# Optimization experiments

Hardware: AMD Instinct MI355X
Metric: run time of the kernel (lower is better)

The kernel has to match this reference:

```python
import jax, jax.numpy as jnp
import numpy as np

N_ENT = 100000   # n_entities
N_REL = 64       # n_relations
E_DIM = 64       # e_dim == r_dim (rel2ent is None)
K = 32           # neighbors per entity
B = 1024         # batch of seed entities
SLOPE = 0.2      # LeakyReLU negative_slope


def _xavier(key, shape, fan_in, fan_out):
    b = (6.0 / (fan_in + fan_out)) ** 0.5
    return jax.random.uniform(key, shape, jnp.float32, -b, b)


def setup_inputs() -> dict:
    key = jax.random.key(0)
    ks = jax.random.split(key, 10)
    E = _xavier(ks[0], (N_ENT, E_DIM), N_ENT, E_DIM)          # entity_embs.weight
    R = _xavier(ks[1], (N_REL, E_DIM), N_REL, E_DIM)          # relation_embs.weight
    att_w1 = _xavier(ks[2], (E_DIM, 2 * E_DIM), 2 * E_DIM, E_DIM)  # attention[0], no bias
    att_w2 = _xavier(ks[3], (E_DIM, E_DIM), E_DIM, E_DIM)          # attention[2], no bias
    att_w3 = _xavier(ks[4], (1, E_DIM), E_DIM, 1)                  # attention[4], no bias
    wx_w = _xavier(ks[5], (E_DIM, E_DIM), E_DIM, E_DIM)            # Wx[0].weight
    wx_b = jnp.zeros((E_DIM,), jnp.float32)                        # Wx[0].bias
    wc_w = _xavier(ks[6], (E_DIM, 2 * E_DIM), 2 * E_DIM, E_DIM)    # W_concat.weight
    wc_b = jnp.zeros((E_DIM,), jnp.float32)                        # W_concat.bias
    entity_idx = jax.random.randint(ks[7], (B,), 0, N_ENT)
    adj_entity = jax.random.randint(ks[8], (N_ENT, K), 0, N_ENT)
    adj_relation = jax.random.randint(ks[9], (N_ENT, K), 0, N_REL)
    return {
        "entity_idx": entity_idx, "adj_entity": adj_entity, "adj_relation": adj_relation,
        "E": E, "R": R, "att_w1": att_w1, "att_w2": att_w2, "att_w3": att_w3,
        "wx_w": wx_w, "wx_b": wx_b, "wc_w": wc_w, "wc_b": wc_b,
    }


def _lookup(W, idx):
    # nn.Embedding(max_norm=1): rows whose L2 norm exceeds 1 are renormalized.
    e = W[idx]
    n = jnp.linalg.norm(e, axis=-1, keepdims=True)
    return e * jnp.where(n > 1.0, 1.0 / (n + 1e-7), 1.0)


def _forward(entity_idx, adj_entity, adj_relation, E, R,
             att_w1, att_w2, att_w3, wx_w, wx_b, wc_w, wc_b):
    leaky = lambda x: jnp.where(x >= 0, x, SLOPE * x)
    # attention MLP on cat([h, r]): split first linear so the broadcast h term
    # is computed once per batch row instead of materializing [B, N, 2e].
    w1h, w1r = att_w1[:, :E_DIM], att_w1[:, E_DIM:]

    def gat(h, r, t):
        # h: [B, e] (broadcast over neighbors), r,t: [B, N, e]
        hid = jax.nn.relu(jnp.einsum('be,fe->bf', h, w1h)[:, None, :]
                          + jnp.einsum('bne,fe->bnf', r, w1r))
        hid = jax.nn.relu(jnp.einsum('bnf,gf->bng', hid, att_w2))
        a = jax.nn.sigmoid(jnp.einsum('bng,og->bno', hid, att_w3)[..., 0])  # [B, N]
        w = jax.nn.softmax(a, axis=-1)
        agg = jnp.einsum('bn,bne->be', w, t)       # softmax-weighted neighbor sum
        return agg @ wx_w.T + wx_b                 # per-head Linear (n_heads=1)

    Bsz = entity_idx.shape[0]
    # hop-1 / hop-2 neighbor index gathers (get_neighbors)
    ent1 = adj_entity[entity_idx]                  # [B, K]
    rel1 = adj_relation[entity_idx]                # [B, K]
    ent2 = adj_entity[ent1].reshape(Bsz, -1)       # [B, K*K]
    rel2 = adj_relation[ent1].reshape(Bsz, -1)     # [B, K*K]

    h = _lookup(E, entity_idx)                     # [B, e]
    t1 = _lookup(E, ent1)                          # [B, K, e]
    t2 = _lookup(E, ent2)                          # [B, K*K, e]
    r1 = _lookup(R, rel1)
    r2 = _lookup(R, rel2)

    # iter 0: seed entity broadcast as head
    v1 = leaky(gat(h, r1, t1))                                      # [B, e]
    emb1 = leaky(jnp.concatenate([h, v1], -1) @ wc_w.T + wc_b)      # aggregate 'concat'
    # iter 1: summed hop-1 neighborhood as head
    hsum = t1.sum(axis=1)                                           # [B, e]
    v2 = leaky(gat(hsum, r2, t2))
    emb2 = leaky(jnp.concatenate([hsum, v2], -1) @ wc_w.T + wc_b)
    # sum_aggregator 'concat': e_u = cat(embs[2], cat(embs[1], embs[0]))
    return jnp.concatenate([emb2, emb1, h], axis=-1)                # [B, 3e]


def reference(entity_idx, adj_entity, adj_relation, E, R,
              att_w1, att_w2, att_w3, wx_w, wx_b, wc_w, wc_b):
    return _forward(entity_idx, adj_entity, adj_relation, E, R,
                    att_w1, att_w2, att_w3, wx_w, wx_b, wc_w, wc_b)
```

## Files before the change

kernel.cpp:

```cpp
#include <hip/hip_runtime.h>

#define SLOPE 0.2f

__device__ __forceinline__ float leaky(float x) { return x >= 0.f ? x : SLOPE * x; }

enum : int {
  OFF_PT   = 0,
  OFF_W2T  = OFF_PT + 4096,
  OFF_A3   = OFF_W2T + 4096,
  OFF_WXT  = OFF_A3 + 64,
  OFF_WXB  = OFF_WXT + 4096,
  OFF_WCT  = OFF_WXB + 64,
  OFF_WCB  = OFF_WCT + 8192,
  OFF_W1HT = OFF_WCB + 64,
  OFF_HQ   = OFF_W1HT + 4096,
  OFF_HSUM = OFF_HQ + 131072,
  OFF_ATAB = OFF_HSUM + 65536,
  OFF_ENT1 = OFF_ATAB + 131072,
  OFF_REL1 = OFF_ENT1 + 32768,
  WS_FLOATS = OFF_REL1 + 32768
};

__global__ __launch_bounds__(256) void k1_prep(
    const float* __restrict__ R, const float* __restrict__ w1,
    const float* __restrict__ w2, const float* __restrict__ w3,
    const float* __restrict__ wxw, const float* __restrict__ wxb,
    const float* __restrict__ wcw, const float* __restrict__ wcb,
    float* __restrict__ ws) {
  __shared__ float Rn[64 * 65];
  int tid = threadIdx.x, wv = tid >> 6, lane = tid & 63;
  for (int r = wv; r < 64; r += 4) {
    float v = R[r * 64 + lane];
    float ss = v * v;
    #pragma unroll
    for (int m = 1; m < 64; m <<= 1) ss += __shfl_xor(ss, m, 64);
    float n = sqrtf(ss);
    float sc = n > 1.f ? 1.f / (n + 1e-7f) : 1.f;
    Rn[r * 65 + lane] = v * sc;
  }
  __syncthreads();
  int gt = blockIdx.x * 256 + tid;
  for (int i = gt; i < 4096; i += 2048) {
    int f = i >> 6, r = i & 63;
    float acc = 0.f;
    #pragma unroll
    for (int e = 0; e < 64; ++e) acc += Rn[r * 65 + e] * w1[f * 128 + 64 + e];
    ws[OFF_PT + f * 64 + r] = acc;
  }
  for (int i = gt; i < 4096; i += 2048) {
    int f = i >> 6, g = i & 63;
    ws[OFF_W2T + i] = w2[g * 64 + f];
  }
  for (int i = gt; i < 4096; i += 2048) {
    int e = i >> 6, f = i & 63;
    ws[OFF_WXT + i]  = wxw[f * 64 + e];
    ws[OFF_W1HT + i] = w1[f * 128 + e];
  }
  for (int i = gt; i < 8192; i += 2048) {
    int e = i >> 6, f = i & 63;
    ws[OFF_WCT + i] = wcw[f * 128 + e];
  }
  if (gt < 64) {
    ws[OFF_A3 + gt]  = w3[gt];
    ws[OFF_WXB + gt] = wxb[gt];
    ws[OFF_WCB + gt] = wcb[gt];
  }
}

__global__ __launch_bounds__(256) void k2_stagea(
    const int* __restrict__ entity_idx, const int* __restrict__ adj_entity,
    const int* __restrict__ adj_relation, const float* __restrict__ E,
    float* __restrict__ ws) {
  __shared__ int s_ent1[32];
  __shared__ float s_h[64], s_hs[64];
  __shared__ float s_part[4][64];
  int b = blockIdx.x, tid = threadIdx.x, wv = tid >> 6, lane = tid & 63;
  int idx = entity_idx[b];
  if (tid < 64) s_h[tid] = E[(long)idx * 64 + tid];
  if (tid >= 64 && tid < 96) {
    int i = tid - 64;
    int e1 = adj_entity[(long)idx * 32 + i];
    int r1 = adj_relation[(long)idx * 32 + i];
    s_ent1[i] = e1;
    ((int*)ws)[OFF_ENT1 + b * 32 + i] = e1;
    ((int*)ws)[OFF_REL1 + b * 32 + i] = r1;
  }
  __syncthreads();
  float hs = 0.f;
  #pragma unroll
  for (int k = 0; k < 8; ++k) hs += E[(long)s_ent1[wv * 8 + k] * 64 + lane];
  s_part[wv][lane] = hs;
  __syncthreads();
  if (tid < 64) {
    float t = s_part[0][tid] + s_part[1][tid] + s_part[2][tid] + s_part[3][tid];
    s_hs[tid] = t;
    ws[OFF_HSUM + b * 64 + tid] = t;
  }
  __syncthreads();
  {
    const float* src = (wv < 2) ? s_h : s_hs;
    int e0 = (wv & 1) * 32;
    float p = 0.f;
    #pragma unroll 8
    for (int e = 0; e < 32; ++e) p += ws[OFF_W1HT + (e0 + e) * 64 + lane] * src[e0 + e];
    s_part[wv][lane] = p;
  }
  __syncthreads();
  if (tid < 64) {
    ws[OFF_HQ + (b * 2 + 0) * 64 + tid] = s_part[0][tid] + s_part[1][tid];
  } else if (tid < 128) {
    int i = tid - 64;
    ws[OFF_HQ + (b * 2 + 1) * 64 + i] = s_part[2][i] + s_part[3][i];
  }
}

__global__ __launch_bounds__(256) void k3_atab(const float* __restrict__ ws,
                                               float* __restrict__ atab) {
  __shared__ float s_hid[64 * 64];
  __shared__ float s_part[4][64];
  int g64 = blockIdx.x;
  int tid = threadIdx.x, rel = tid & 63;
  int wv = __builtin_amdgcn_readfirstlane(tid >> 6);
  const float* hq  = ws + OFF_HQ + g64 * 64;
  const float* PT  = ws + OFF_PT;
  const float* W2T = ws + OFF_W2T;
  const float* A3  = ws + OFF_A3;
  #pragma unroll
  for (int i = 0; i < 16; ++i) {
    int f = wv * 16 + i;
    s_hid[f * 64 + rel] = fmaxf(hq[f] + PT[f * 64 + rel], 0.f);
  }
  __syncthreads();
  float acc[16];
  #pragma unroll
  for (int i = 0; i < 16; ++i) acc[i] = 0.f;
  int g0 = wv * 16;
  #pragma unroll 4
  for (int f = 0; f < 64; ++f) {
    float hv = s_hid[f * 64 + rel];
    const float* w = W2T + f * 64 + g0;
    #pragma unroll
    for (int i = 0; i < 16; ++i) acc[i] += w[i] * hv;
  }
  float s = 0.f;
  #pragma unroll
  for (int i = 0; i < 16; ++i) s += A3[g0 + i] * fmaxf(acc[i], 0.f);
  s_part[wv][rel] = s;
  __syncthreads();
  if (tid < 64) {
    float t = s_part[0][tid] + s_part[1][tid] + s_part[2][tid] + s_part[3][tid];
    float a = 1.f / (1.f + __expf(-t));
    atab[g64 * 64 + tid] = __expf(a);
  }
}

__global__ __launch_bounds__(256) void k4_agg(
    const int* __restrict__ entity_idx, const int* __restrict__ adj_entity,
    const int* __restrict__ adj_relation, const float* __restrict__ E,
    const float* __restrict__ ws, float* __restrict__ out) {
  __shared__ int s_ent1[32], s_rel1[32];
  __shared__ float s_at1[64], s_at2[64];
  __shared__ int s_ei[1024];
  __shared__ float s_w[1024];
  __shared__ float s_accA[4][64];
  __shared__ float s_accB[4][64];
  __shared__ float s_agg1[64], s_agg2[64], s_v1[64], s_v2[64], s_h[64], s_hs[64];
  __shared__ float s_L1, s_L2;
  int b = blockIdx.x, tid = threadIdx.x, wv = tid >> 6, lane = tid & 63;
  int sub = lane >> 4, eg = lane & 15;
  const float4* E4 = (const float4*)E;

  if (tid < 32) {
    s_ent1[tid] = ((const int*)ws)[OFF_ENT1 + b * 32 + tid];
    s_rel1[tid] = ((const int*)ws)[OFF_REL1 + b * 32 + tid];
  }
  if (tid >= 64 && tid < 128) {
    int i = tid - 64;
    s_at1[i] = ws[OFF_ATAB + (b * 2 + 0) * 64 + i];
    s_at2[i] = ws[OFF_ATAB + (b * 2 + 1) * 64 + i];
  }
  if (tid >= 128 && tid < 192) {
    int i = tid - 128;
    s_h[i]  = E[(long)entity_idx[b] * 64 + i];
    s_hs[i] = ws[OFF_HSUM + b * 64 + i];
  }
  if (tid == 0) s_L2 = 0.f;
  __syncthreads();

  float wsum = 0.f;
  #pragma unroll
  for (int i = 0; i < 4; ++i) {
    int n = tid + i * 256;
    int j = n >> 5, i2 = n & 31;
    long base = (long)s_ent1[j] * 32 + i2;
    int ei = adj_entity[base];
    int ri = adj_relation[base];
    float wgt = s_at2[ri];
    s_ei[n] = ei;
    s_w[n] = wgt;
    wsum += wgt;
  }
  #pragma unroll
  for (int m = 1; m < 64; m <<= 1) wsum += __shfl_xor(wsum, m, 64);
  if (lane == 0) atomicAdd(&s_L2, wsum);

  if (tid < 32) {
    float w = s_at1[s_rel1[tid]];
    #pragma unroll
    for (int m = 1; m < 32; m <<= 1) w += __shfl_xor(w, m, 64);
    if (tid == 0) s_L1 = w;
  }

  {
    float4 acc = {0.f, 0.f, 0.f, 0.f};
    #pragma unroll
    for (int i = 0; i < 2; ++i) {
      int n = i * 16 + wv * 4 + sub;
      float wgt = s_at1[s_rel1[n]];
      float4 v = E4[(long)s_ent1[n] * 16 + eg];
      acc.x += wgt * v.x; acc.y += wgt * v.y; acc.z += wgt * v.z; acc.w += wgt * v.w;
    }
    #pragma unroll
    for (int m = 16; m < 64; m <<= 1) {
      acc.x += __shfl_xor(acc.x, m, 64); acc.y += __shfl_xor(acc.y, m, 64);
      acc.z += __shfl_xor(acc.z, m, 64); acc.w += __shfl_xor(acc.w, m, 64);
    }
    if (sub == 0) {
      s_accA[wv][eg * 4 + 0] = acc.x; s_accA[wv][eg * 4 + 1] = acc.y;
      s_accA[wv][eg * 4 + 2] = acc.z; s_accA[wv][eg * 4 + 3] = acc.w;
    }
  }

  {
    float4 acc = {0.f, 0.f, 0.f, 0.f};
    #pragma unroll 8
    for (int i = 0; i < 64; ++i) {
      int n = i * 16 + wv * 4 + sub;
      float wgt = s_w[n];
      float4 v = E4[(long)s_ei[n] * 16 + eg];
      acc.x += wgt * v.x; acc.y += wgt * v.y; acc.z += wgt * v.z; acc.w += wgt * v.w;
    }
    #pragma unroll
    for (int m = 16; m < 64; m <<= 1) {
      acc.x += __shfl_xor(acc.x, m, 64); acc.y += __shfl_xor(acc.y, m, 64);
      acc.z += __shfl_xor(acc.z, m, 64); acc.w += __shfl_xor(acc.w, m, 64);
    }
    if (sub == 0) {
      s_accB[wv][eg * 4 + 0] = acc.x; s_accB[wv][eg * 4 + 1] = acc.y;
      s_accB[wv][eg * 4 + 2] = acc.z; s_accB[wv][eg * 4 + 3] = acc.w;
    }
  }
  __syncthreads();

  if (tid < 64) {
    float a = s_accA[0][tid] + s_accA[1][tid] + s_accA[2][tid] + s_accA[3][tid];
    s_agg1[tid] = a / s_L1;
  } else if (tid < 128) {
    int i = tid - 64;
    float a = s_accB[0][i] + s_accB[1][i] + s_accB[2][i] + s_accB[3][i];
    s_agg2[i] = a / s_L2;
  }
  __syncthreads();

  {
    const float* src = (wv < 2) ? s_agg1 : s_agg2;
    int e0 = (wv & 1) * 32;
    float p = 0.f;
    #pragma unroll 8
    for (int e = 0; e < 32; ++e)
      p += ws[OFF_WXT + (e0 + e) * 64 + lane] * src[e0 + e];
    s_accA[wv][lane] = p;
  }
  __syncthreads();
  if (tid < 64) {
    s_v1[tid] = leaky(ws[OFF_WXB + tid] + s_accA[0][tid] + s_accA[1][tid]);
  } else if (tid < 128) {
    int i = tid - 64;
    s_v2[i] = leaky(ws[OFF_WXB + i] + s_accA[2][i] + s_accA[3][i]);
  }
  __syncthreads();

  {
    const float* src = (wv == 0) ? s_h : (wv == 1) ? s_v1 : (wv == 2) ? s_hs : s_v2;
    int e0 = (wv & 1) * 64;
    float p = 0.f;
    #pragma unroll 8
    for (int e = 0; e < 64; ++e)
      p += ws[OFF_WCT + (e0 + e) * 64 + lane] * src[e];
    s_accB[wv][lane] = p;
  }
  __syncthreads();
  if (tid < 64) {
    float o = ws[OFF_WCB + tid] + s_accB[0][tid] + s_accB[1][tid];
    out[b * 192 + 64 + tid]  = leaky(o);
    out[b * 192 + 128 + tid] = s_h[tid];
  } else if (tid < 128) {
    int i = tid - 64;
    float o = ws[OFF_WCB + i] + s_accB[2][i] + s_accB[3][i];
    out[b * 192 + i] = leaky(o);
  }
}

extern "C" void kernel_launch(void* const* d_in, const int* in_sizes, int n_in,
                              void* d_out, int out_size, void* d_ws, size_t ws_size,
                              hipStream_t stream) {
  const int* entity_idx   = (const int*)d_in[0];
  const int* adj_entity   = (const int*)d_in[1];
  const int* adj_relation = (const int*)d_in[2];
  const float* E          = (const float*)d_in[3];
  const float* R          = (const float*)d_in[4];
  const float* att_w1     = (const float*)d_in[5];
  const float* att_w2     = (const float*)d_in[6];
  const float* att_w3     = (const float*)d_in[7];
  const float* wx_w       = (const float*)d_in[8];
  const float* wx_b       = (const float*)d_in[9];
  const float* wc_w       = (const float*)d_in[10];
  const float* wc_b       = (const float*)d_in[11];
  float* out              = (float*)d_out;
  float* ws               = (float*)d_ws;

  hipLaunchKernelGGL(k1_prep, dim3(8), dim3(256), 0, stream,
                     R, att_w1, att_w2, att_w3, wx_w, wx_b, wc_w, wc_b, ws);
  hipLaunchKernelGGL(k2_stagea, dim3(1024), dim3(256), 0, stream,
                     entity_idx, adj_entity, adj_relation, E, ws);
  hipLaunchKernelGGL(k3_atab, dim3(2048), dim3(256), 0, stream,
                     ws, ws + OFF_ATAB);
  hipLaunchKernelGGL(k4_agg, dim3(1024), dim3(256), 0, stream,
                     entity_idx, adj_entity, adj_relation, E, ws, out);
}
```

Measured before the change: 166.4 us.

## Fuse stage-A, attention table, and aggregation kernels into one per-seed kernel

Merges k2_stagea, k3_atab and k4_agg into a single kernel with one block per seed entity. Intermediates (hq, hsum, attention tables, hop-1 indices) stay in shared memory instead of round-tripping through the workspace. Hop-1 neighbor embeddings are cached in LDS and reused for both the sum and the weighted aggregation, which removes a second gather. The trade-off is that the attention MLP now runs on 1024 blocks instead of 2048, each doing both heads serially, and shared memory use grows to about 34KB per block, which may lower occupancy.

```diff
diff --git a/kernel.cpp b/kernel.cpp
--- a/kernel.cpp
+++ b/kernel.cpp
@@ -13,12 +13,7 @@
   OFF_WCT  = OFF_WXB + 64,
   OFF_WCB  = OFF_WCT + 8192,
   OFF_W1HT = OFF_WCB + 64,
-  OFF_HQ   = OFF_W1HT + 4096,
-  OFF_HSUM = OFF_HQ + 131072,
-  OFF_ATAB = OFF_HSUM + 65536,
-  OFF_ENT1 = OFF_ATAB + 131072,
-  OFF_REL1 = OFF_ENT1 + 32768,
-  WS_FLOATS = OFF_REL1 + 32768
+  WS_FLOATS = OFF_W1HT + 4096
 };
 
 __global__ __launch_bounds__(256) void k1_prep(
@@ -67,169 +62,128 @@
   }
 }
 
-__global__ __launch_bounds__(256) void k2_stagea(
-    const int* __restrict__ entity_idx, const int* __restrict__ adj_entity,
-    const int* __restrict__ adj_relation, const float* __restrict__ E,
-    float* __restrict__ ws) {
-  __shared__ int s_ent1[32];
-  __shared__ float s_h[64], s_hs[64];
-  __shared__ float s_part[4][64];
-  int b = blockIdx.x, tid = threadIdx.x, wv = tid >> 6, lane = tid & 63;
-  int idx = entity_idx[b];
-  if (tid < 64) s_h[tid] = E[(long)idx * 64 + tid];
-  if (tid >= 64 && tid < 96) {
-    int i = tid - 64;
-    int e1 = adj_entity[(long)idx * 32 + i];
-    int r1 = adj_relation[(long)idx * 32 + i];
-    s_ent1[i] = e1;
-    ((int*)ws)[OFF_ENT1 + b * 32 + i] = e1;
-    ((int*)ws)[OFF_REL1 + b * 32 + i] = r1;
-  }
-  __syncthreads();
-  float hs = 0.f;
-  #pragma unroll
-  for (int k = 0; k < 8; ++k) hs += E[(long)s_ent1[wv * 8 + k] * 64 + lane];
-  s_part[wv][lane] = hs;
-  __syncthreads();
-  if (tid < 64) {
-    float t = s_part[0][tid] + s_part[1][tid] + s_part[2][tid] + s_part[3][tid];
-    s_hs[tid] = t;
-    ws[OFF_HSUM + b * 64 + tid] = t;
-  }
-  __syncthreads();
-  {
-    const float* src = (wv < 2) ? s_h : s_hs;
-    int e0 = (wv & 1) * 32;
-    float p = 0.f;
-    #pragma unroll 8
-    for (int e = 0; e < 32; ++e) p += ws[OFF_W1HT + (e0 + e) * 64 + lane] * src[e0 + e];
-    s_part[wv][lane] = p;
-  }
-  __syncthreads();
-  if (tid < 64) {
-    ws[OFF_HQ + (b * 2 + 0) * 64 + tid] = s_part[0][tid] + s_part[1][tid];
-  } else if (tid < 128) {
-    int i = tid - 64;
-    ws[OFF_HQ + (b * 2 + 1) * 64 + i] = s_part[2][i] + s_part[3][i];
-  }
-}
-
-__global__ __launch_bounds__(256) void k3_atab(const float* __restrict__ ws,
-                                               float* __restrict__ atab) {
-  __shared__ float s_hid[64 * 64];
-  __shared__ float s_part[4][64];
-  int g64 = blockIdx.x;
-  int tid = threadIdx.x, rel = tid & 63;
-  int wv = __builtin_amdgcn_readfirstlane(tid >> 6);
-  const float* hq  = ws + OFF_HQ + g64 * 64;
-  const float* PT  = ws + OFF_PT;
-  const float* W2T = ws + OFF_W2T;
-  const float* A3  = ws + OFF_A3;
-  #pragma unroll
-  for (int i = 0; i < 16; ++i) {
-    int f = wv * 16 + i;
-    s_hid[f * 64 + rel] = fmaxf(hq[f] + PT[f * 64 + rel], 0.f);
-  }
-  __syncthreads();
-  float acc[16];
-  #pragma unroll
-  for (int i = 0; i < 16; ++i) acc[i] = 0.f;
-  int g0 = wv * 16;
-  #pragma unroll 4
-  for (int f = 0; f < 64; ++f) {
-    float hv = s_hid[f * 64 + rel];
-    const float* w = W2T + f * 64 + g0;
-    #pragma unroll
-    for (int i = 0; i < 16; ++i) acc[i] += w[i] * hv;
-  }
-  float s = 0.f;
-  #pragma unroll
-  for (int i = 0; i < 16; ++i) s += A3[g0 + i] * fmaxf(acc[i], 0.f);
-  s_part[wv][rel] = s;
-  __syncthreads();
-  if (tid < 64) {
-    float t = s_part[0][tid] + s_part[1][tid] + s_part[2][tid] + s_part[3][tid];
-    float a = 1.f / (1.f + __expf(-t));
-    atab[g64 * 64 + tid] = __expf(a);
-  }
-}
-
-__global__ __launch_bounds__(256) void k4_agg(
+__global__ __launch_bounds__(256) void k_main(
     const int* __restrict__ entity_idx, const int* __restrict__ adj_entity,
     const int* __restrict__ adj_relation, const float* __restrict__ E,
     const float* __restrict__ ws, float* __restrict__ out) {
-  __shared__ int s_ent1[32], s_rel1[32];
-  __shared__ float s_at1[64], s_at2[64];
-  __shared__ int s_ei[1024];
+  __shared__ float s_t1[32 * 64];
+  __shared__ float s_pt[64 * 64];
+  __shared__ float s_partA[4][64], s_partB[4][64];
+  __shared__ int   s_ent1[32], s_rel1[32];
+  __shared__ int   s_ei[1024];
   __shared__ float s_w[1024];
-  __shared__ float s_accA[4][64];
-  __shared__ float s_accB[4][64];
-  __shared__ float s_agg1[64], s_agg2[64], s_v1[64], s_v2[64], s_h[64], s_hs[64];
+  __shared__ float s_h[64], s_hs[64], s_hq1[64], s_hq2[64];
+  __shared__ float s_at1[64], s_at2[64], s_agg1[64], s_agg2[64], s_v1[64], s_v2[64];
   __shared__ float s_L1, s_L2;
   int b = blockIdx.x, tid = threadIdx.x, wv = tid >> 6, lane = tid & 63;
   int sub = lane >> 4, eg = lane & 15;
   const float4* E4 = (const float4*)E;
-
-  if (tid < 32) {
-    s_ent1[tid] = ((const int*)ws)[OFF_ENT1 + b * 32 + tid];
-    s_rel1[tid] = ((const int*)ws)[OFF_REL1 + b * 32 + tid];
-  }
-  if (tid >= 64 && tid < 128) {
-    int i = tid - 64;
-    s_at1[i] = ws[OFF_ATAB + (b * 2 + 0) * 64 + i];
-    s_at2[i] = ws[OFF_ATAB + (b * 2 + 1) * 64 + i];
-  }
-  if (tid >= 128 && tid < 192) {
-    int i = tid - 128;
-    s_h[i]  = E[(long)entity_idx[b] * 64 + i];
-    s_hs[i] = ws[OFF_HSUM + b * 64 + i];
+  int idx = entity_idx[b];
+
+  if (tid < 64) s_h[tid] = E[(long)idx * 64 + tid];
+  if (tid >= 64 && tid < 96) {
+    int i = tid - 64;
+    s_ent1[i] = adj_entity[(long)idx * 32 + i];
+    s_rel1[i] = adj_relation[(long)idx * 32 + i];
   }
   if (tid == 0) s_L2 = 0.f;
-  __syncthreads();
-
-  float wsum = 0.f;
-  #pragma unroll
-  for (int i = 0; i < 4; ++i) {
-    int n = tid + i * 256;
-    int j = n >> 5, i2 = n & 31;
-    long base = (long)s_ent1[j] * 32 + i2;
-    int ei = adj_entity[base];
-    int ri = adj_relation[base];
-    float wgt = s_at2[ri];
-    s_ei[n] = ei;
-    s_w[n] = wgt;
-    wsum += wgt;
-  }
-  #pragma unroll
-  for (int m = 1; m < 64; m <<= 1) wsum += __shfl_xor(wsum, m, 64);
-  if (lane == 0) atomicAdd(&s_L2, wsum);
-
+  for (int j = tid; j < 4096; j += 256) s_pt[j] = ws[OFF_PT + j];
+  __syncthreads();
+
+  {
+    float hs = 0.f;
+    #pragma unroll
+    for (int k = 0; k < 8; ++k) {
+      int n = wv * 8 + k;
+      float v = E[(long)s_ent1[n] * 64 + lane];
+      s_t1[n * 64 + lane] = v;
+      hs += v;
+    }
+    s_partA[wv][lane] = hs;
+  }
+  __syncthreads();
+  if (tid < 64)
+    s_hs[tid] = s_partA[0][tid] + s_partA[1][tid] + s_partA[2][tid] + s_partA[3][tid];
+  __syncthreads();
+
+  {
+    const float* src = (wv < 2) ? s_h : s_hs;
+    int e0 = (wv & 1) * 32;
+    float p = 0.f;
+    #pragma unroll 8
+    for (int e = 0; e < 32; ++e) p += ws[OFF_W1HT + (e0 + e) * 64 + lane] * src[e0 + e];
+    s_partA[wv][lane] = p;
+  }
+  __syncthreads();
+  if (tid < 64) s_hq1[tid] = s_partA[0][tid] + s_partA[1][tid];
+  else if (tid < 128) { int i = tid - 64; s_hq2[i] = s_partA[2][i] + s_partA[3][i]; }
+  __syncthreads();
+
+  {
+    int swv = __builtin_amdgcn_readfirstlane(wv);
+    const float* W2T = ws + OFF_W2T;
+    const float* A3  = ws + OFF_A3;
+    float acc1[16], acc2[16];
+    #pragma unroll
+    for (int i = 0; i < 16; ++i) { acc1[i] = 0.f; acc2[i] = 0.f; }
+    int g0 = swv * 16;
+    #pragma unroll 2
+    for (int f = 0; f < 64; ++f) {
+      float ptv = s_pt[f * 64 + lane];
+      float h1 = fmaxf(s_hq1[f] + ptv, 0.f);
+      float h2 = fmaxf(s_hq2[f] + ptv, 0.f);
+      const float* w = W2T + f * 64 + g0;
+      #pragma unroll
+      for (int i = 0; i < 16; ++i) { acc1[i] += w[i] * h1; acc2[i] += w[i] * h2; }
+    }
+    float s1 = 0.f, s2 = 0.f;
+    #pragma unroll
+    for (int i = 0; i < 16; ++i) {
+      float a3 = A3[g0 + i];
+      s1 += a3 * fmaxf(acc1[i], 0.f);
+      s2 += a3 * fmaxf(acc2[i], 0.f);
+    }
+    s_partA[wv][lane] = s1;
+    s_partB[wv][lane] = s2;
+  }
+  __syncthreads();
+  if (tid < 64) {
+    float t = s_partA[0][tid] + s_partA[1][tid] + s_partA[2][tid] + s_partA[3][tid];
+    float a = 1.f / (1.f + __expf(-t));
+    s_at1[tid] = __expf(a);
+  } else if (tid < 128) {
+    int i = tid - 64;
+    float t = s_partB[0][i] + s_partB[1][i] + s_partB[2][i] + s_partB[3][i];
+    float a = 1.f / (1.f + __expf(-t));
+    s_at2[i] = __expf(a);
+  }
+  __syncthreads();
+
+  {
+    float wsum = 0.f;
+    #pragma unroll
+    for (int i = 0; i < 4; ++i) {
+      int n = tid + i * 256;
+      int j = n >> 5, i2 = n & 31;
+      long base = (long)s_ent1[j] * 32 + i2;
+      int ei = adj_entity[base];
+      int ri = adj_relation[base];
+      float wgt = s_at2[ri];
+      s_ei[n] = ei;
+      s_w[n] = wgt;
+      wsum += wgt;
+    }
+    #pragma unroll
+    for (int m = 1; m < 64; m <<= 1) wsum += __shfl_xor(wsum, m, 64);
+    if (lane == 0) atomicAdd(&s_L2, wsum);
+  }
   if (tid < 32) {
     float w = s_at1[s_rel1[tid]];
     #pragma unroll
     for (int m = 1; m < 32; m <<= 1) w += __shfl_xor(w, m, 64);
     if (tid == 0) s_L1 = w;
   }
-
-  {
-    float4 acc = {0.f, 0.f, 0.f, 0.f};
-    #pragma unroll
-    for (int i = 0; i < 2; ++i) {
-      int n = i * 16 + wv * 4 + sub;
-      float wgt = s_at1[s_rel1[n]];
-      float4 v = E4[(long)s_ent1[n] * 16 + eg];
-      acc.x += wgt * v.x; acc.y += wgt * v.y; acc.z += wgt * v.z; acc.w += wgt * v.w;
-    }
-    #pragma unroll
-    for (int m = 16; m < 64; m <<= 1) {
-      acc.x += __shfl_xor(acc.x, m, 64); acc.y += __shfl_xor(acc.y, m, 64);
-      acc.z += __shfl_xor(acc.z, m, 64); acc.w += __shfl_xor(acc.w, m, 64);
-    }
-    if (sub == 0) {
-      s_accA[wv][eg * 4 + 0] = acc.x; s_accA[wv][eg * 4 + 1] = acc.y;
-      s_accA[wv][eg * 4 + 2] = acc.z; s_accA[wv][eg * 4 + 3] = acc.w;
-    }
-  }
+  __syncthreads();
 
   {
     float4 acc = {0.f, 0.f, 0.f, 0.f};
@@ -246,18 +200,26 @@
       acc.z += __shfl_xor(acc.z, m, 64); acc.w += __shfl_xor(acc.w, m, 64);
     }
     if (sub == 0) {
-      s_accB[wv][eg * 4 + 0] = acc.x; s_accB[wv][eg * 4 + 1] = acc.y;
-      s_accB[wv][eg * 4 + 2] = acc.z; s_accB[wv][eg * 4 + 3] = acc.w;
-    }
-  }
-  __syncthreads();
-
-  if (tid < 64) {
-    float a = s_accA[0][tid] + s_accA[1][tid] + s_accA[2][tid] + s_accA[3][tid];
+      s_partB[wv][eg * 4 + 0] = acc.x; s_partB[wv][eg * 4 + 1] = acc.y;
+      s_partB[wv][eg * 4 + 2] = acc.z; s_partB[wv][eg * 4 + 3] = acc.w;
+    }
+  }
+  {
+    float a1 = 0.f;
+    #pragma unroll
+    for (int k = 0; k < 8; ++k) {
+      int n = wv * 8 + k;
+      a1 += s_at1[s_rel1[n]] * s_t1[n * 64 + lane];
+    }
+    s_partA[wv][lane] = a1;
+  }
+  __syncthreads();
+  if (tid < 64) {
+    float a = s_partA[0][tid] + s_partA[1][tid] + s_partA[2][tid] + s_partA[3][tid];
     s_agg1[tid] = a / s_L1;
   } else if (tid < 128) {
     int i = tid - 64;
-    float a = s_accB[0][i] + s_accB[1][i] + s_accB[2][i] + s_accB[3][i];
+    float a = s_partB[0][i] + s_partB[1][i] + s_partB[2][i] + s_partB[3][i];
     s_agg2[i] = a / s_L2;
   }
   __syncthreads();
@@ -269,14 +231,14 @@
     #pragma unroll 8
     for (int e = 0; e < 32; ++e)
       p += ws[OFF_WXT + (e0 + e) * 64 + lane] * src[e0 + e];
-    s_accA[wv][lane] = p;
-  }
-  __syncthreads();
-  if (tid < 64) {
-    s_v1[tid] = leaky(ws[OFF_WXB + tid] + s_accA[0][tid] + s_accA[1][tid]);
-  } else if (tid < 128) {
-    int i = tid - 64;
-    s_v2[i] = leaky(ws[OFF_WXB + i] + s_accA[2][i] + s_accA[3][i]);
+    s_partA[wv][lane] = p;
+  }
+  __syncthreads();
+  if (tid < 64) {
+    s_v1[tid] = leaky(ws[OFF_WXB + tid] + s_partA[0][tid] + s_partA[1][tid]);
+  } else if (tid < 128) {
+    int i = tid - 64;
+    s_v2[i] = leaky(ws[OFF_WXB + i] + s_partA[2][i] + s_partA[3][i]);
   }
   __syncthreads();
 
@@ -287,16 +249,16 @@
     #pragma unroll 8
     for (int e = 0; e < 64; ++e)
       p += ws[OFF_WCT + (e0 + e) * 64 + lane] * src[e];
-    s_accB[wv][lane] = p;
-  }
-  __syncthreads();
-  if (tid < 64) {
-    float o = ws[OFF_WCB + tid] + s_accB[0][tid] + s_accB[1][tid];
+    s_partB[wv][lane] = p;
+  }
+  __syncthreads();
+  if (tid < 64) {
+    float o = ws[OFF_WCB + tid] + s_partB[0][tid] + s_partB[1][tid];
     out[b * 192 + 64 + tid]  = leaky(o);
     out[b * 192 + 128 + tid] = s_h[tid];
   } else if (tid < 128) {
     int i = tid - 64;
-    float o = ws[OFF_WCB + i] + s_accB[2][i] + s_accB[3][i];
+    float o = ws[OFF_WCB + i] + s_partB[2][i] + s_partB[3][i];
     out[b * 192 + i] = leaky(o);
   }
 }
@@ -321,10 +283,6 @@
 
   hipLaunchKernelGGL(k1_prep, dim3(8), dim3(256), 0, stream,
                      R, att_w1, att_w2, att_w3, wx_w, wx_b, wc_w, wc_b, ws);
-  hipLaunchKernelGGL(k2_stagea, dim3(1024), dim3(256), 0, stream,
-                     entity_idx, adj_entity, adj_relation, E, ws);
-  hipLaunchKernelGGL(k3_atab, dim3(2048), dim3(256), 0, stream,
-                     ws, ws + OFF_ATAB);
-  hipLaunchKernelGGL(k4_agg, dim3(1024), dim3(256), 0, stream,
+  hipLaunchKernelGGL(k_main, dim3(1024), dim3(256), 0, stream,
                      entity_idx, adj_entity, adj_relation, E, ws, out);
 }
```

After: 162.9 us. 2.1% less time.
